# Kernel optimization log

Hardware: AMD Instinct MI355X
Metric: run time of the kernel (lower is better)

## Reference

```python
import jax, jax.numpy as jnp
import numpy as np

EPS_IN = 1e-5   # InstanceNorm2d default eps
EPS_VAR = 1e-6  # clamp on attention variance

def instance_norm(x):
    # x: (b, c, h, w); affine=False, biased variance over spatial dims
    mean = jnp.mean(x, axis=(2, 3), keepdims=True)
    var = jnp.var(x, axis=(2, 3), keepdims=True)
    return (x - mean) * jax.lax.rsqrt(var + EPS_IN)

def setup_inputs() -> dict:
    key = jax.random.key(0)
    k1, k2, k3, k4 = jax.random.split(key, 4)
    shp = (4, 512, 64, 64)
    return {
        "c_x": jax.random.normal(k1, shp, dtype=jnp.float32),
        "s_x": jax.random.normal(k2, shp, dtype=jnp.float32),
        "c_1x": jax.random.normal(k3, shp, dtype=jnp.float32),
        "s_1x": jax.random.normal(k4, shp, dtype=jnp.float32),
    }

def reference(c_x, s_x, c_1x, s_1x):
    b, v_dim, h, w = c_x.shape
    hw = h * w
    # Q: (b, hw, qk), K: (b, qk, hw), V: (b, hw, v)
    Q = instance_norm(c_1x).reshape(b, -1, hw).transpose(0, 2, 1)
    K = instance_norm(s_1x).reshape(b, -1, s_1x.shape[2] * s_1x.shape[3])
    V = s_x.reshape(b, v_dim, -1).transpose(0, 2, 1)
    # attention over spatial tokens
    A = jax.nn.softmax(jnp.einsum('bqc,bck->bqk', Q, K), axis=-1)
    M = jnp.einsum('bqk,bkv->bqv', A, V)              # weighted mean
    Var = jnp.einsum('bqk,bkv->bqv', A, V * V) - M * M  # weighted variance
    S = jnp.sqrt(jnp.clip(Var, EPS_VAR, None))
    # back to (b, v, h, w)
    M = M.reshape(b, h, w, -1).transpose(0, 3, 1, 2)
    S = S.reshape(b, h, w, -1).transpose(0, 3, 1, 2)
    return S * instance_norm(c_x) + M
```

## Files before the change

kernel.cpp:

```cpp
#include <hip/hip_runtime.h>
#include <cmath>


#define B_  4
#define C_  512
#define HW_ 4096

typedef _Float16 f16;
typedef _Float16 f16x8 __attribute__((ext_vector_type(8)));
typedef float    f32x4 __attribute__((ext_vector_type(4)));

__device__ __forceinline__ f32x4 mfma16(f16x8 a, f16x8 b, f32x4 c) {
  return __builtin_amdgcn_mfma_f32_16x16x32_f16(a, b, c, 0, 0, 0);
}
__device__ __forceinline__ void g2l16(const f16* g, f16* l) {
  __builtin_amdgcn_global_load_lds(
      (const __attribute__((address_space(1))) void*)g,
      (__attribute__((address_space(3))) void*)l, 16, 0, 0);
}

__global__ __launch_bounds__(256) void k_stats(
    const float* __restrict__ cx, const float* __restrict__ c1,
    const float* __restrict__ s1,
    float2* __restrict__ cxs, float2* __restrict__ c1s, float2* __restrict__ s1s) {
  int c = blockIdx.x, b = blockIdx.y, t = blockIdx.z;
  const float* src = (t == 0 ? cx : (t == 1 ? c1 : s1)) + (size_t)(b * C_ + c) * HW_;
  float s = 0.f, q = 0.f;
  const float4* src4 = (const float4*)src;
  for (int i = threadIdx.x; i < HW_ / 4; i += 256) {
    float4 v = src4[i];
    s += v.x + v.y + v.z + v.w;
    q += v.x * v.x + v.y * v.y + v.z * v.z + v.w * v.w;
  }
#pragma unroll
  for (int off = 1; off < 64; off <<= 1) {
    s += __shfl_xor(s, off);
    q += __shfl_xor(q, off);
  }
  __shared__ float ss[4], sq[4];
  int wv = threadIdx.x >> 6;
  if ((threadIdx.x & 63) == 0) { ss[wv] = s; sq[wv] = q; }
  __syncthreads();
  if (threadIdx.x == 0) {
    float S = ss[0] + ss[1] + ss[2] + ss[3];
    float Q = sq[0] + sq[1] + sq[2] + sq[3];
    float mean = S * (1.f / HW_);
    float var = Q * (1.f / HW_) - mean * mean;
    float2 r;
    r.x = mean;
    r.y = rsqrtf(var + 1e-5f);
    (t == 0 ? cxs : (t == 1 ? c1s : s1s))[b * C_ + c] = r;
  }
}

__global__ __launch_bounds__(256) void k_prept(
    const float* __restrict__ src, const float2* __restrict__ st,
    f16* __restrict__ dst) {
  int pb = blockIdx.x * 64, cb = blockIdx.y * 64, b = blockIdx.z;
  __shared__ float t[64][65];
  int tj = threadIdx.x & 63, tr = threadIdx.x >> 6;
#pragma unroll 4
  for (int p = 0; p < 16; ++p) {
    int cl = p * 4 + tr;
    float2 mr = st[b * C_ + cb + cl];
    float v = src[(size_t)(b * C_ + cb + cl) * HW_ + pb + tj];
    t[cl][tj] = (v - mr.x) * mr.y;
  }
  __syncthreads();
#pragma unroll 4
  for (int p = 0; p < 16; ++p) {
    int pr = p * 4 + tr;
    dst[(size_t)(b * HW_ + pb + pr) * C_ + cb + tj] = (f16)t[tj][pr];
  }
}

__global__ __launch_bounds__(256) void k_prepv(const float* __restrict__ src,
                                               f16* __restrict__ dst) {
  int gid = blockIdx.x * 256 + threadIdx.x;
  const float4* s = (const float4*)src + (size_t)gid * 2;
  float4 v0 = s[0], v1 = s[1];
  f16x8 v = {(f16)v0.x, (f16)v0.y, (f16)v0.z, (f16)v0.w,
             (f16)v1.x, (f16)v1.y, (f16)v1.z, (f16)v1.w};
  *(f16x8*)(dst + (size_t)gid * 8) = v;
}

__global__ __launch_bounds__(256, 2) void k_qk(
    const f16* __restrict__ Qt, const f16* __restrict__ Kt,
    f16* __restrict__ E, float2* __restrict__ mlpart,
    int qspan, int qt128, int npair) {
  int id = blockIdx.x, pair, kt;
  if ((npair & 7) == 0) {
    int xcd = id & 7, j = id >> 3, qrs = npair >> 3;
    pair = xcd * qrs + (j % qrs);
    kt = j / qrs;
  } else {
    pair = id >> 4;
    kt = id & 15;
  }
  int bz = pair / qt128, qt = pair - bz * qt128;

  const f16* Aq = Qt + ((size_t)(bz * qspan + qt * 128)) * C_;
  const f16* Bk = Kt + (size_t)bz * HW_ * C_ + (size_t)kt * 256 * C_;
  f16* Eb = E + ((size_t)(bz * qspan + qt * 128)) * HW_ + kt * 256;
  float2* mlb = mlpart + ((size_t)(bz * qspan + qt * 128)) * 16 + kt;

  __shared__ __align__(16) union ShQK {
    struct { f16 As[128 * 32]; f16 Bs[256 * 32]; } s;
    f16 ebuf[32 * 272];
  } sh;
  __shared__ float sred[2][128];
  f16* As = sh.s.As;
  f16* Bs = sh.s.Bs;

  int t = threadIdx.x, wave = t >> 6, lane = t & 63, lq = lane & 15, quad = lane >> 4;
  int wy = wave >> 1, wx = wave & 1;
  int srow = t >> 2, scol = (t & 3) * 8;

  f32x4 acc[4][8];
#pragma unroll
  for (int mt = 0; mt < 4; ++mt)
#pragma unroll
    for (int nt = 0; nt < 8; ++nt) acc[mt][nt] = (f32x4){0, 0, 0, 0};

  for (int kc = 0; kc < 16; ++kc) {
    __syncthreads();
    g2l16(Aq + (size_t)srow * C_ + kc * 32 + scol, As + t * 8);
    g2l16(Aq + (size_t)(srow + 64) * C_ + kc * 32 + scol, As + 2048 + t * 8);
#pragma unroll
    for (int i = 0; i < 4; ++i)
      g2l16(Bk + (size_t)(srow + 64 * i) * C_ + kc * 32 + scol,
            Bs + i * 2048 + t * 8);
    __syncthreads();
    f16x8 af[4], bf[8];
#pragma unroll
    for (int mt = 0; mt < 4; ++mt)
      af[mt] = *(const f16x8*)(As + (wy * 64 + mt * 16 + lq) * 32 + quad * 8);
#pragma unroll
    for (int nt = 0; nt < 8; ++nt)
      bf[nt] = *(const f16x8*)(Bs + (wx * 128 + nt * 16 + lq) * 32 + quad * 8);
#pragma unroll
    for (int mt = 0; mt < 4; ++mt)
#pragma unroll
      for (int nt = 0; nt < 8; ++nt)
        acc[mt][nt] = mfma16(af[mt], bf[nt], acc[mt][nt]);
  }

#pragma unroll
  for (int mt = 0; mt < 4; ++mt)
#pragma unroll
    for (int r = 0; r < 4; ++r) {
      float v = -1e30f;
#pragma unroll
      for (int nt = 0; nt < 8; ++nt) v = fmaxf(v, acc[mt][nt][r]);
#pragma unroll
      for (int msk = 1; msk < 16; msk <<= 1) v = fmaxf(v, __shfl_xor(v, msk));
      if (lq == 0) sred[wx][wy * 64 + mt * 16 + quad * 4 + r] = v;
    }
  __syncthreads();
  float mrow[4][4];
#pragma unroll
  for (int mt = 0; mt < 4; ++mt)
#pragma unroll
    for (int r = 0; r < 4; ++r) {
      int rr = wy * 64 + mt * 16 + quad * 4 + r;
      mrow[mt][r] = fmaxf(sred[0][rr], sred[1][rr]);
    }

  float rsum[4][4];
#pragma unroll
  for (int mt = 0; mt < 4; ++mt)
#pragma unroll
    for (int r = 0; r < 4; ++r) rsum[mt][r] = 0.f;

#pragma unroll
  for (int mt = 0; mt < 4; ++mt) {
    __syncthreads();
#pragma unroll
    for (int nt = 0; nt < 8; ++nt) {
      f32x4 v = acc[mt][nt];
#pragma unroll
      for (int r = 0; r < 4; ++r) {
        float e = __expf(v[r] - mrow[mt][r]);
        rsum[mt][r] += e;
        sh.ebuf[(wy * 16 + quad * 4 + r) * 272 + wx * 128 + nt * 16 + lq] = (f16)e;
      }
    }
    __syncthreads();
#pragma unroll
    for (int i = 0; i < 4; ++i) {
      int idx = i * 256 + t;
      int rl = idx >> 5, cs = (idx & 31) * 8;
      f16x8 v8 = *(const f16x8*)(sh.ebuf + rl * 272 + cs);
      int grow = (rl >> 4) * 64 + mt * 16 + (rl & 15);
      *(f16x8*)(Eb + (size_t)grow * HW_ + cs) = v8;
    }
  }

#pragma unroll
  for (int mt = 0; mt < 4; ++mt)
#pragma unroll
    for (int r = 0; r < 4; ++r) {
      float v = rsum[mt][r];
#pragma unroll
      for (int msk = 1; msk < 16; msk <<= 1) v += __shfl_xor(v, msk);
      if (lq == 0) sred[wx][wy * 64 + mt * 16 + quad * 4 + r] = v;
    }
  __syncthreads();
  if (wx == 0 && lq == 0) {
#pragma unroll
    for (int mt = 0; mt < 4; ++mt)
#pragma unroll
      for (int r = 0; r < 4; ++r) {
        int rr = wy * 64 + mt * 16 + quad * 4 + r;
        mlb[(size_t)rr * 16] = make_float2(mrow[mt][r], sred[0][rr] + sred[1][rr]);
      }
  }
}

__global__ __launch_bounds__(256) void k_red(const float2* __restrict__ mlpart,
                                             float* __restrict__ alpha) {
  int row = blockIdx.x * 256 + threadIdx.x;
  const float2* p = mlpart + (size_t)row * 16;
  float2 loc[16];
  float m = -1e30f;
#pragma unroll
  for (int i = 0; i < 16; ++i) {
    loc[i] = p[i];
    m = fmaxf(m, loc[i].x);
  }
  float l = 0.f;
#pragma unroll
  for (int i = 0; i < 16; ++i) l += loc[i].y * __expf(loc[i].x - m);
  float invl = 1.f / l;
#pragma unroll
  for (int i = 0; i < 16; ++i)
    alpha[(size_t)row * 16 + i] = __expf(loc[i].x - m) * invl;
}

__global__ __launch_bounds__(256, 2) void k_pv(
    const f16* __restrict__ P, const float* __restrict__ alphaG,
    const f16* __restrict__ V, const float* __restrict__ cx,
    const float2* __restrict__ cxs, float* __restrict__ out,
    int qspan, int qbase, int qt128) {
  int npairs = (int)gridDim.x >> 2;
  int id = blockIdx.x, pair, ct;
  if ((npairs & 7) == 0) {
    int x = id & 7, j = id >> 3, ppx = npairs >> 3;
    pair = x * ppx + (j >> 2);
    ct = j & 3;
  } else {
    pair = id >> 2;
    ct = id & 3;
  }
  int bz = pair / qt128, qt = pair - bz * qt128;

  const f16* Ap = P + ((size_t)(bz * qspan + qt * 128)) * HW_;
  const f16* Bv = V + ((size_t)(bz * C_ + ct * 128)) * HW_;

  __shared__ __align__(16) f16 As[128 * 32], Bs[128 * 32];
  __shared__ float Al[128 * 17];

  int t = threadIdx.x, wave = t >> 6, lane = t & 63, lq = lane & 15, quad = lane >> 4;
  int wy = wave >> 1, wx = wave & 1;
  int srow = t >> 2, scol = (t & 3) * 8;

  {
    const float* ag = alphaG + ((size_t)(bz * qspan + qt * 128)) * 16;
#pragma unroll
    for (int i = 0; i < 8; ++i) {
      int e = i * 256 + t;
      Al[(e >> 4) * 17 + (e & 15)] = ag[e];
    }
  }

  f32x4 accM[4][4], accM2[4][4];
#pragma unroll
  for (int mt = 0; mt < 4; ++mt)
#pragma unroll
    for (int nt = 0; nt < 4; ++nt) {
      accM[mt][nt] = (f32x4){0, 0, 0, 0};
      accM2[mt][nt] = (f32x4){0, 0, 0, 0};
    }

  for (int kc = 0; kc < 128; ++kc) {
    __syncthreads();
    g2l16(Ap + (size_t)srow * HW_ + kc * 32 + scol, As + t * 8);
    g2l16(Ap + (size_t)(srow + 64) * HW_ + kc * 32 + scol, As + 2048 + t * 8);
    g2l16(Bv + (size_t)srow * HW_ + kc * 32 + scol, Bs + t * 8);
    g2l16(Bv + (size_t)(srow + 64) * HW_ + kc * 32 + scol, Bs + 2048 + t * 8);
    __syncthreads();

    int ktl = kc >> 3;
    f16x8 af[4], bf[4], bf2[4];
#pragma unroll
    for (int mt = 0; mt < 4; ++mt) {
      af[mt] = *(const f16x8*)(As + (wy * 64 + mt * 16 + lq) * 32 + quad * 8);
      f16 a = (f16)Al[(wy * 64 + mt * 16 + lq) * 17 + ktl];
      af[mt] = af[mt] * a;
    }
#pragma unroll
    for (int nt = 0; nt < 4; ++nt) {
      bf[nt] = *(const f16x8*)(Bs + (wx * 64 + nt * 16 + lq) * 32 + quad * 8);
      bf2[nt] = bf[nt] * bf[nt];
    }
#pragma unroll
    for (int mt = 0; mt < 4; ++mt)
#pragma unroll
      for (int nt = 0; nt < 4; ++nt) {
        accM[mt][nt] = mfma16(af[mt], bf[nt], accM[mt][nt]);
        accM2[mt][nt] = mfma16(af[mt], bf2[nt], accM2[mt][nt]);
      }
  }

  int chbase = ct * 128 + wx * 64;
#pragma unroll
  for (int mt = 0; mt < 4; ++mt) {
    int q0 = qbase + qt * 128 + wy * 64 + mt * 16 + quad * 4;
#pragma unroll
    for (int nt = 0; nt < 4; ++nt) {
      int c = chbase + nt * 16 + lq;
      float2 st = cxs[bz * C_ + c];
      size_t base = ((size_t)bz * C_ + c) * HW_ + q0;
      float4 cv = *(const float4*)(cx + base);
      f32x4 m1 = accM[mt][nt], m2 = accM2[mt][nt];
      float4 o;
      o.x = sqrtf(fmaxf(m2[0] - m1[0] * m1[0], 1e-6f)) * ((cv.x - st.x) * st.y) + m1[0];
      o.y = sqrtf(fmaxf(m2[1] - m1[1] * m1[1], 1e-6f)) * ((cv.y - st.x) * st.y) + m1[1];
      o.z = sqrtf(fmaxf(m2[2] - m1[2] * m1[2], 1e-6f)) * ((cv.z - st.x) * st.y) + m1[2];
      o.w = sqrtf(fmaxf(m2[3] - m1[3] * m1[3], 1e-6f)) * ((cv.w - st.x) * st.y) + m1[3];
      *(float4*)(out + base) = o;
    }
  }
}

extern "C" void kernel_launch(void* const* d_in, const int* in_sizes, int n_in,
                              void* d_out, int out_size, void* d_ws,
                              size_t ws_size, hipStream_t stream) {
  const float* c_x = (const float*)d_in[0];
  const float* s_x = (const float*)d_in[1];
  const float* c1x = (const float*)d_in[2];
  const float* s1x = (const float*)d_in[3];
  float* out = (float*)d_out;

  char* ws = (char*)d_ws;
  size_t o = 0;
  f16* Qt = (f16*)(ws + o);  o += (size_t)B_ * HW_ * C_ * 2;
  f16* Kt = (f16*)(ws + o);  o += (size_t)B_ * HW_ * C_ * 2;
  f16* Vh = (f16*)(ws + o);  o += (size_t)B_ * HW_ * C_ * 2;
  float2* cxs = (float2*)(ws + o); o += B_ * C_ * sizeof(float2);
  float2* c1s = (float2*)(ws + o); o += B_ * C_ * sizeof(float2);
  float2* s1s = (float2*)(ws + o); o += B_ * C_ * sizeof(float2);
  size_t fixed = (o + 255) & ~(size_t)255;

  const size_t per_row = (size_t)HW_ * 2 + 16 * 8 + 16 * 4;
  struct Cfg { int nb, qs; };
  const Cfg cfgs[5] = {{4, 4096}, {1, 4096}, {1, 2048}, {1, 1024}, {1, 512}};
  Cfg cfg = cfgs[4];
  for (int i = 0; i < 5; ++i) {
    size_t rows = (size_t)cfgs[i].nb * cfgs[i].qs;
    if (fixed + rows * per_row <= ws_size) { cfg = cfgs[i]; break; }
  }
  const int nb = cfg.nb, qspan = cfg.qs, qt128 = qspan / 128;
  const int npair = nb * qt128;
  const size_t rows = (size_t)nb * qspan;
  f16* E = (f16*)(ws + fixed);
  float2* mlpart = (float2*)(ws + fixed + rows * HW_ * 2);
  float* alpha = (float*)(ws + fixed + rows * HW_ * 2 + rows * 16 * 8);

  k_stats<<<dim3(C_, B_, 3), 256, 0, stream>>>(c_x, c1x, s1x, cxs, c1s, s1s);
  k_prept<<<dim3(HW_ / 64, C_ / 64, B_), 256, 0, stream>>>(c1x, c1s, Qt);
  k_prept<<<dim3(HW_ / 64, C_ / 64, B_), 256, 0, stream>>>(s1x, s1s, Kt);
  k_prepv<<<dim3(B_ * C_ * HW_ / 8 / 256), 256, 0, stream>>>(s_x, Vh);

  for (int b0 = 0; b0 < B_; b0 += nb) {
    for (int qb = 0; qb < HW_; qb += qspan) {
      const f16* Qtp = Qt + ((size_t)b0 * HW_ + qb) * C_;
      const f16* Ktp = Kt + (size_t)b0 * HW_ * C_;
      const f16* Vp = Vh + (size_t)b0 * C_ * HW_;
      const float* cxp = c_x + (size_t)b0 * C_ * HW_;
      const float2* cxsp = cxs + b0 * C_;
      float* outp = out + (size_t)b0 * C_ * HW_;

      k_qk<<<dim3((unsigned)(npair * 16)), 256, 0, stream>>>(
          Qtp, Ktp, E, mlpart, qspan, qt128, npair);
      k_red<<<dim3((unsigned)(rows / 256)), 256, 0, stream>>>(mlpart, alpha);
      k_pv<<<dim3((unsigned)(npair * 4)), 256, 0, stream>>>(
          E, alpha, Vp, cxp, cxsp, outp, qspan, qb, qt128);
    }
  }
}
```

Before: 423.9 us.

## Drop cross-wave softmax reductions and batch E stores; merge prep launches

k_qk now records a per-wave (max,sum) partial for each 128-column half, so there are 32 partials per row instead of 16. This removes the LDS cross-wave max and sum reductions and most of the barriers. The exp tile is written into a full 128x272 LDS buffer and stored once at the end instead of in four synchronized chunks. k_red and k_pv are widened to handle 32 partials. k_stats now uses one wave per channel without LDS, and the Q/K preparation is merged into a single launch. The trade-off is a larger LDS footprint in k_qk, which may lower occupancy, plus more partial-statistics traffic.

New measurement: 434.7 us. +2.5%, slower.

```diff
diff --git a/kernel.cpp b/kernel.cpp
--- a/kernel.cpp
+++ b/kernel.cpp
@@ -23,12 +23,14 @@
     const float* __restrict__ cx, const float* __restrict__ c1,
     const float* __restrict__ s1,
     float2* __restrict__ cxs, float2* __restrict__ c1s, float2* __restrict__ s1s) {
-  int c = blockIdx.x, b = blockIdx.y, t = blockIdx.z;
+  int wave = threadIdx.x >> 6, lane = threadIdx.x & 63;
+  int c = blockIdx.x * 4 + wave, b = blockIdx.y, t = blockIdx.z;
   const float* src = (t == 0 ? cx : (t == 1 ? c1 : s1)) + (size_t)(b * C_ + c) * HW_;
+  const float4* src4 = (const float4*)src;
   float s = 0.f, q = 0.f;
-  const float4* src4 = (const float4*)src;
-  for (int i = threadIdx.x; i < HW_ / 4; i += 256) {
-    float4 v = src4[i];
+#pragma unroll
+  for (int j = 0; j < 16; ++j) {
+    float4 v = src4[lane + j * 64];
     s += v.x + v.y + v.z + v.w;
     q += v.x * v.x + v.y * v.y + v.z * v.z + v.w * v.w;
   }
@@ -37,15 +39,9 @@
     s += __shfl_xor(s, off);
     q += __shfl_xor(q, off);
   }
-  __shared__ float ss[4], sq[4];
-  int wv = threadIdx.x >> 6;
-  if ((threadIdx.x & 63) == 0) { ss[wv] = s; sq[wv] = q; }
-  __syncthreads();
-  if (threadIdx.x == 0) {
-    float S = ss[0] + ss[1] + ss[2] + ss[3];
-    float Q = sq[0] + sq[1] + sq[2] + sq[3];
-    float mean = S * (1.f / HW_);
-    float var = Q * (1.f / HW_) - mean * mean;
+  if (lane == 0) {
+    float mean = s * (1.f / HW_);
+    float var = q * (1.f / HW_) - mean * mean;
     float2 r;
     r.x = mean;
     r.y = rsqrtf(var + 1e-5f);
@@ -54,9 +50,14 @@
 }
 
 __global__ __launch_bounds__(256) void k_prept(
-    const float* __restrict__ src, const float2* __restrict__ st,
-    f16* __restrict__ dst) {
-  int pb = blockIdx.x * 64, cb = blockIdx.y * 64, b = blockIdx.z;
+    const float* __restrict__ c1x, const float* __restrict__ s1x,
+    const float2* __restrict__ c1s, const float2* __restrict__ s1s,
+    f16* __restrict__ Qt, f16* __restrict__ Kt) {
+  int pb = blockIdx.x * 64, cb = blockIdx.y * 64;
+  int b = blockIdx.z >> 1, which = blockIdx.z & 1;
+  const float* src = which ? s1x : c1x;
+  const float2* st = which ? s1s : c1s;
+  f16* dst = which ? Kt : Qt;
   __shared__ float t[64][65];
   int tj = threadIdx.x & 63, tr = threadIdx.x >> 6;
 #pragma unroll 4
@@ -102,13 +103,12 @@
   const f16* Aq = Qt + ((size_t)(bz * qspan + qt * 128)) * C_;
   const f16* Bk = Kt + (size_t)bz * HW_ * C_ + (size_t)kt * 256 * C_;
   f16* Eb = E + ((size_t)(bz * qspan + qt * 128)) * HW_ + kt * 256;
-  float2* mlb = mlpart + ((size_t)(bz * qspan + qt * 128)) * 16 + kt;
+  float2* mlb = mlpart + ((size_t)(bz * qspan + qt * 128)) * 32 + kt * 2;
 
   __shared__ __align__(16) union ShQK {
     struct { f16 As[128 * 32]; f16 Bs[256 * 32]; } s;
-    f16 ebuf[32 * 272];
+    f16 ebuf[128 * 272];
   } sh;
-  __shared__ float sred[2][128];
   f16* As = sh.s.As;
   f16* Bs = sh.s.Bs;
 
@@ -145,6 +145,7 @@
         acc[mt][nt] = mfma16(af[mt], bf[nt], acc[mt][nt]);
   }
 
+  float mrow[4][4], rsum[4][4];
 #pragma unroll
   for (int mt = 0; mt < 4; ++mt)
 #pragma unroll
@@ -154,27 +155,14 @@
       for (int nt = 0; nt < 8; ++nt) v = fmaxf(v, acc[mt][nt][r]);
 #pragma unroll
       for (int msk = 1; msk < 16; msk <<= 1) v = fmaxf(v, __shfl_xor(v, msk));
-      if (lq == 0) sred[wx][wy * 64 + mt * 16 + quad * 4 + r] = v;
-    }
+      mrow[mt][r] = v;
+      rsum[mt][r] = 0.f;
+    }
+
   __syncthreads();
-  float mrow[4][4];
-#pragma unroll
-  for (int mt = 0; mt < 4; ++mt)
-#pragma unroll
-    for (int r = 0; r < 4; ++r) {
-      int rr = wy * 64 + mt * 16 + quad * 4 + r;
-      mrow[mt][r] = fmaxf(sred[0][rr], sred[1][rr]);
-    }
-
-  float rsum[4][4];
-#pragma unroll
-  for (int mt = 0; mt < 4; ++mt)
-#pragma unroll
-    for (int r = 0; r < 4; ++r) rsum[mt][r] = 0.f;
-
-#pragma unroll
-  for (int mt = 0; mt < 4; ++mt) {
-    __syncthreads();
+
+#pragma unroll
+  for (int mt = 0; mt < 4; ++mt)
 #pragma unroll
     for (int nt = 0; nt < 8; ++nt) {
       f32x4 v = acc[mt][nt];
@@ -182,19 +170,10 @@
       for (int r = 0; r < 4; ++r) {
         float e = __expf(v[r] - mrow[mt][r]);
         rsum[mt][r] += e;
-        sh.ebuf[(wy * 16 + quad * 4 + r) * 272 + wx * 128 + nt * 16 + lq] = (f16)e;
+        sh.ebuf[(wy * 64 + mt * 16 + quad * 4 + r) * 272 +
+                wx * 128 + nt * 16 + lq] = (f16)e;
       }
     }
-    __syncthreads();
-#pragma unroll
-    for (int i = 0; i < 4; ++i) {
-      int idx = i * 256 + t;
-      int rl = idx >> 5, cs = (idx & 31) * 8;
-      f16x8 v8 = *(const f16x8*)(sh.ebuf + rl * 272 + cs);
-      int grow = (rl >> 4) * 64 + mt * 16 + (rl & 15);
-      *(f16x8*)(Eb + (size_t)grow * HW_ + cs) = v8;
-    }
-  }
 
 #pragma unroll
   for (int mt = 0; mt < 4; ++mt)
@@ -203,38 +182,40 @@
       float v = rsum[mt][r];
 #pragma unroll
       for (int msk = 1; msk < 16; msk <<= 1) v += __shfl_xor(v, msk);
-      if (lq == 0) sred[wx][wy * 64 + mt * 16 + quad * 4 + r] = v;
+      if (lq == 0) {
+        int rr = wy * 64 + mt * 16 + quad * 4 + r;
+        mlb[(size_t)rr * 32 + wx] = make_float2(mrow[mt][r], v);
+      }
     }
   __syncthreads();
-  if (wx == 0 && lq == 0) {
-#pragma unroll
-    for (int mt = 0; mt < 4; ++mt)
-#pragma unroll
-      for (int r = 0; r < 4; ++r) {
-        int rr = wy * 64 + mt * 16 + quad * 4 + r;
-        mlb[(size_t)rr * 16] = make_float2(mrow[mt][r], sred[0][rr] + sred[1][rr]);
-      }
+
+#pragma unroll
+  for (int i = 0; i < 16; ++i) {
+    int idx = i * 256 + t;
+    int rl = idx >> 5, cs = (idx & 31) * 8;
+    f16x8 v8 = *(const f16x8*)(sh.ebuf + rl * 272 + cs);
+    *(f16x8*)(Eb + (size_t)rl * HW_ + cs) = v8;
   }
 }
 
 __global__ __launch_bounds__(256) void k_red(const float2* __restrict__ mlpart,
                                              float* __restrict__ alpha) {
   int row = blockIdx.x * 256 + threadIdx.x;
-  const float2* p = mlpart + (size_t)row * 16;
-  float2 loc[16];
+  const float2* p = mlpart + (size_t)row * 32;
+  float2 loc[32];
   float m = -1e30f;
 #pragma unroll
-  for (int i = 0; i < 16; ++i) {
+  for (int i = 0; i < 32; ++i) {
     loc[i] = p[i];
     m = fmaxf(m, loc[i].x);
   }
   float l = 0.f;
 #pragma unroll
-  for (int i = 0; i < 16; ++i) l += loc[i].y * __expf(loc[i].x - m);
+  for (int i = 0; i < 32; ++i) l += loc[i].y * __expf(loc[i].x - m);
   float invl = 1.f / l;
 #pragma unroll
-  for (int i = 0; i < 16; ++i)
-    alpha[(size_t)row * 16 + i] = __expf(loc[i].x - m) * invl;
+  for (int i = 0; i < 32; ++i)
+    alpha[(size_t)row * 32 + i] = __expf(loc[i].x - m) * invl;
 }
 
 __global__ __launch_bounds__(256, 2) void k_pv(
@@ -258,18 +239,18 @@
   const f16* Bv = V + ((size_t)(bz * C_ + ct * 128)) * HW_;
 
   __shared__ __align__(16) f16 As[128 * 32], Bs[128 * 32];
-  __shared__ float Al[128 * 17];
+  __shared__ float Al[128 * 33];
 
   int t = threadIdx.x, wave = t >> 6, lane = t & 63, lq = lane & 15, quad = lane >> 4;
   int wy = wave >> 1, wx = wave & 1;
   int srow = t >> 2, scol = (t & 3) * 8;
 
   {
-    const float* ag = alphaG + ((size_t)(bz * qspan + qt * 128)) * 16;
-#pragma unroll
-    for (int i = 0; i < 8; ++i) {
+    const float* ag = alphaG + ((size_t)(bz * qspan + qt * 128)) * 32;
+#pragma unroll
+    for (int i = 0; i < 16; ++i) {
       int e = i * 256 + t;
-      Al[(e >> 4) * 17 + (e & 15)] = ag[e];
+      Al[(e >> 5) * 33 + (e & 31)] = ag[e];
     }
   }
 
@@ -290,12 +271,12 @@
     g2l16(Bv + (size_t)(srow + 64) * HW_ + kc * 32 + scol, Bs + 2048 + t * 8);
     __syncthreads();
 
-    int ktl = kc >> 3;
+    int ktl = kc >> 2;
     f16x8 af[4], bf[4], bf2[4];
 #pragma unroll
     for (int mt = 0; mt < 4; ++mt) {
       af[mt] = *(const f16x8*)(As + (wy * 64 + mt * 16 + lq) * 32 + quad * 8);
-      f16 a = (f16)Al[(wy * 64 + mt * 16 + lq) * 17 + ktl];
+      f16 a = (f16)Al[(wy * 64 + mt * 16 + lq) * 33 + ktl];
       af[mt] = af[mt] * a;
     }
 #pragma unroll
@@ -352,7 +333,7 @@
   float2* s1s = (float2*)(ws + o); o += B_ * C_ * sizeof(float2);
   size_t fixed = (o + 255) & ~(size_t)255;
 
-  const size_t per_row = (size_t)HW_ * 2 + 16 * 8 + 16 * 4;
+  const size_t per_row = (size_t)HW_ * 2 + 32 * 8 + 32 * 4;
   struct Cfg { int nb, qs; };
   const Cfg cfgs[5] = {{4, 4096}, {1, 4096}, {1, 2048}, {1, 1024}, {1, 512}};
   Cfg cfg = cfgs[4];
@@ -365,11 +346,11 @@
   const size_t rows = (size_t)nb * qspan;
   f16* E = (f16*)(ws + fixed);
   float2* mlpart = (float2*)(ws + fixed + rows * HW_ * 2);
-  float* alpha = (float*)(ws + fixed + rows * HW_ * 2 + rows * 16 * 8);
-
-  k_stats<<<dim3(C_, B_, 3), 256, 0, stream>>>(c_x, c1x, s1x, cxs, c1s, s1s);
-  k_prept<<<dim3(HW_ / 64, C_ / 64, B_), 256, 0, stream>>>(c1x, c1s, Qt);
-  k_prept<<<dim3(HW_ / 64, C_ / 64, B_), 256, 0, stream>>>(s1x, s1s, Kt);
+  float* alpha = (float*)(ws + fixed + rows * HW_ * 2 + rows * 32 * 8);
+
+  k_stats<<<dim3(C_ / 4, B_, 3), 256, 0, stream>>>(c_x, c1x, s1x, cxs, c1s, s1s);
+  k_prept<<<dim3(HW_ / 64, C_ / 64, 2 * B_), 256, 0, stream>>>(c1x, s1x, c1s,
+                                                               s1s, Qt, Kt);
   k_prepv<<<dim3(B_ * C_ * HW_ / 8 / 256), 256, 0, stream>>>(s_x, Vh);
 
   for (int b0 = 0; b0 < B_; b0 += nb) {
```
